# Kernel optimization log

Hardware: AMD Instinct MI355X
Metric: run time of the kernel (lower is better)

Reference implementation:

```python
import jax, jax.numpy as jnp
import numpy as np

HEADS = 8

def setup_inputs() -> dict:
    key = jax.random.key(0)
    k1, k2, k3 = jax.random.split(key, 3)
    B, C, L = 8, 512, 4096
    dim_head = 64
    hidden = HEADS * dim_head  # 512
    x = jax.random.normal(k1, (B, C, L), dtype=jnp.float32)
    # Conv1d(dim, hidden*3, 1, bias=False) -> weight [hidden*3, dim]
    w_qkv = jax.random.normal(k2, (hidden * 3, C), dtype=jnp.float32) * 0.02
    # Conv1d(hidden, dim, 1) -> weight [dim, hidden], bias [dim]
    w_out = jax.random.normal(k3, (C, hidden), dtype=jnp.float32) * 0.02
    b_out = jnp.zeros((C,), dtype=jnp.float32)
    return {"x": x, "w_qkv": w_qkv, "w_out": w_out, "b_out": b_out}

def reference(x, w_qkv, w_out, b_out):
    B, C, L = x.shape
    # 1x1 Conv1d == channel matmul
    qkv = jnp.einsum('oc,bcl->bol', w_qkv, x)            # [B, 3*H*dh, L]
    qkv = qkv.reshape(B, 3, HEADS, -1, L)                # qkv outermost, then heads, then c
    q, k, v = qkv[:, 0], qkv[:, 1], qkv[:, 2]            # each [B, H, dh, L]
    k = jax.nn.softmax(k, axis=-1)                       # softmax over sequence
    context = jnp.einsum('bhdn,bhen->bhde', k, v)        # [B, H, dh, dh]
    out = jnp.einsum('bhde,bhdn->bhen', context, q)      # [B, H, dh, L]
    out = out.reshape(B, -1, L)                          # [B, H*dh, L]
    return jnp.einsum('oc,bcl->bol', w_out, out) + b_out[None, :, None]
```

## Files before the change

kernel.cpp:

```cpp
#include <hip/hip_runtime.h>
#include <hip/hip_bf16.h>


typedef __bf16 bf16x8 __attribute__((ext_vector_type(8)));
typedef __bf16 bf16x4 __attribute__((ext_vector_type(4)));
typedef float  f32x4  __attribute__((ext_vector_type(4)));

#define B_  8
#define L_  4096
#define C_  512

#define GLD_LDS16(g, l)                                             \
    __builtin_amdgcn_global_load_lds(                               \
        (const __attribute__((address_space(1))) void*)(g),         \
        (__attribute__((address_space(3))) void*)(l), 16, 0, 0)

__global__ __launch_bounds__(256) void prep_all(const float* __restrict__ x,
                                                __hip_bfloat16* __restrict__ xt,
                                                const float* __restrict__ wqkv_f,
                                                __hip_bfloat16* __restrict__ wkv_b,
                                                __hip_bfloat16* __restrict__ wqT,
                                                float* __restrict__ ctx) {
    __shared__ float tile[64 * 132];
    int blk = blockIdx.x;
    int t = threadIdx.x;
    if (blk < 2048) {
        int b = blk >> 8, rem = blk & 255;
        int l0 = (rem & 31) * 128, c0 = (rem >> 5) * 64;
        const float* xp = x + ((size_t)b * C_ + c0) * L_ + l0;
#pragma unroll
        for (int p = 0; p < 8; p++) {
            int i = p * 8 + (t >> 5);
            int j = (t & 31) * 4;
            float4 vv = *(const float4*)(xp + (size_t)i * L_ + j);
            *(float4*)&tile[i * 132 + j] = vv;
        }
        __syncthreads();
        unsigned short* xo = (unsigned short*)xt + ((size_t)b * L_ + l0) * C_ + c0;
#pragma unroll
        for (int qq = 0; qq < 8; qq++) {
            int l = qq * 16 + (t >> 4);
            int cg = (t & 15) * 4;
            bf16x4 ov;
#pragma unroll
            for (int k = 0; k < 4; k++) ov[k] = (__bf16)tile[(cg + k) * 132 + l];
            *(bf16x4*)(xo + (size_t)l * C_ + cg) = ov;
        }
    } else if (blk < 4096) {
        int i = (blk - 2048) * 256 + t;
        wkv_b[i] = __float2bfloat16(wqkv_f[512 * 512 + i]);
    } else if (blk < 4352) {
        int tb = blk - 4096;
        int r0 = (tb >> 4) * 32, c0 = (tb & 15) * 32;
        int tx = t & 31, ty = t >> 5;
        for (int r = 0; r < 32; r += 8)
            tile[(ty + r) * 33 + tx] = wqkv_f[(size_t)(r0 + ty + r) * 512 + c0 + tx];
        __syncthreads();
        for (int r = 0; r < 32; r += 8)
            wqT[(size_t)(c0 + ty + r) * 512 + r0 + tx] = __float2bfloat16(tile[tx * 33 + ty + r]);
    } else {
        int i = (blk - 4352) * 256 + t;
        ctx[i] = 0.f;
    }
}

template <int MODE>
__global__ __launch_bounds__(256) void gemm_bt(
    const __hip_bfloat16* __restrict__ A, const __hip_bfloat16* __restrict__ Bt,
    size_t strideA, size_t strideB, int M, int N, int K,
    __hip_bfloat16* __restrict__ kb, __hip_bfloat16* __restrict__ vb,
    __hip_bfloat16* __restrict__ obf,
    float* __restrict__ outb, const float* __restrict__ bias) {
    __shared__ alignas(16) unsigned short As[128 * 64];
    __shared__ alignas(16) unsigned short Bs[128 * 64];

    int b = blockIdx.z;
    int m0 = blockIdx.y * 128, n0 = blockIdx.x * 128;
    const __hip_bfloat16* Ab = A + strideA * (size_t)b;
    const __hip_bfloat16* Bb = Bt + strideB * (size_t)b;

    int t = threadIdx.x;
    int lane = t & 63, wv = t >> 6;
    int l16 = lane & 15, q4 = lane >> 4;
    int wr = (wv >> 1) * 64, wc = (wv & 1) * 64;

    int srow = lane >> 3;
    int swz  = ((lane & 7) ^ srow) * 8;

    const __hip_bfloat16* gA[4];
    const __hip_bfloat16* gB[4];
    unsigned short* lA[4];
    unsigned short* lB[4];
#pragma unroll
    for (int c = 0; c < 4; c++) {
        int r = wv * 32 + c * 8;
        gA[c] = Ab + (size_t)(m0 + r + srow) * K + swz;
        gB[c] = Bb + (size_t)(n0 + r + srow) * K + swz;
        lA[c] = &As[r * 64];
        lB[c] = &Bs[r * 64];
    }

    int gsel0 = ((q4) ^ (l16 & 7)) * 8;
    int gsel1 = ((4 + q4) ^ (l16 & 7)) * 8;
    int rA = (wr + l16) * 64;
    int rB = (wc + l16) * 64;

    f32x4 acc[4][4] = {};

    for (int k0 = 0; k0 < K; k0 += 64) {
        __syncthreads();
#pragma unroll
        for (int c = 0; c < 4; c++) {
            GLD_LDS16(gA[c] + k0, lA[c]);
            GLD_LDS16(gB[c] + k0, lB[c]);
        }
        __syncthreads();

        bf16x8 af[4], bfr[4];
#pragma unroll
        for (int i = 0; i < 4; i++) {
            af[i]  = *(const bf16x8*)&As[rA + i * 1024 + gsel0];
            bfr[i] = *(const bf16x8*)&Bs[rB + i * 1024 + gsel0];
        }
#pragma unroll
        for (int i = 0; i < 4; i++)
#pragma unroll
            for (int j = 0; j < 4; j++)
                acc[i][j] = __builtin_amdgcn_mfma_f32_16x16x32_bf16(af[i], bfr[j], acc[i][j], 0, 0, 0);
#pragma unroll
        for (int i = 0; i < 4; i++) {
            af[i]  = *(const bf16x8*)&As[rA + i * 1024 + gsel1];
            bfr[i] = *(const bf16x8*)&Bs[rB + i * 1024 + gsel1];
        }
#pragma unroll
        for (int i = 0; i < 4; i++)
#pragma unroll
            for (int j = 0; j < 4; j++)
                acc[i][j] = __builtin_amdgcn_mfma_f32_16x16x32_bf16(af[i], bfr[j], acc[i][j], 0, 0, 0);
    }

#pragma unroll
    for (int i = 0; i < 4; i++)
#pragma unroll
        for (int j = 0; j < 4; j++)
#pragma unroll
            for (int r = 0; r < 4; r++) {
                int row = m0 + wr + i * 16 + q4 * 4 + r;
                int col = n0 + wc + j * 16 + l16;
                float val = acc[i][j][r];
                if (MODE == 1) {
                    int part = row >> 9, od = row & 511;
                    size_t idx = ((size_t)b * 512 + od) * (size_t)N + col;
                    __hip_bfloat16 cv = __float2bfloat16(val);
                    if (part == 0) kb[idx] = cv;
                    else           vb[idx] = cv;
                } else if (MODE == 3) {
                    obf[((size_t)b * 512 + row) * (size_t)N + col] = __float2bfloat16(val);
                } else {
                    outb[((size_t)b * 512 + row) * (size_t)N + col] = val + bias[row];
                }
            }
}

__global__ __launch_bounds__(256) void rowstat(const __hip_bfloat16* __restrict__ kin,
                                               float* __restrict__ mrow,
                                               float* __restrict__ isrow) {
    int row = blockIdx.x;
    const unsigned short* kp = (const unsigned short*)kin + (size_t)row * L_;
    __shared__ float buf[L_];
    __shared__ float red[8];
    int t = threadIdx.x, lane = t & 63, wv = t >> 6;
    float m = -1e30f;
    for (int i0 = t * 8; i0 < L_; i0 += 256 * 8) {
        bf16x8 kv = *(const bf16x8*)(kp + i0);
#pragma unroll
        for (int j = 0; j < 8; j++) {
            float xx = (float)kv[j];
            buf[i0 + j] = xx;
            m = fmaxf(m, xx);
        }
    }
    for (int o = 32; o; o >>= 1) m = fmaxf(m, __shfl_xor(m, o, 64));
    if (lane == 0) red[wv] = m;
    __syncthreads();
    m = fmaxf(fmaxf(red[0], red[1]), fmaxf(red[2], red[3]));
    float s = 0.f;
    for (int i = t; i < L_; i += 256) s += __expf(buf[i] - m);
    for (int o = 32; o; o >>= 1) s += __shfl_xor(s, o, 64);
    if (lane == 0) red[4 + wv] = s;
    __syncthreads();
    if (t == 0) {
        s = red[4] + red[5] + red[6] + red[7];
        mrow[row] = m;
        isrow[row] = 1.0f / s;
    }
}

__global__ __launch_bounds__(256) void ctx_kernel(const __hip_bfloat16* __restrict__ kraw,
                                                  const float* __restrict__ mrow,
                                                  const float* __restrict__ isrow,
                                                  const __hip_bfloat16* __restrict__ v,
                                                  float* __restrict__ ctx) {
    int kc = blockIdx.x, h = blockIdx.y, b = blockIdx.z;
    int t = threadIdx.x, lane = t & 63, wv = t >> 6;
    int l16 = lane & 15, q4 = lane >> 4;
    const __hip_bfloat16* ka = kraw + ((size_t)b * 512 + h * 64) * L_;
    const __hip_bfloat16* va = v + ((size_t)b * 512 + h * 64) * L_;
    int rbase = b * 512 + h * 64;
    float mr[4], ir[4];
#pragma unroll
    for (int i = 0; i < 4; i++) {
        mr[i] = mrow[rbase + i * 16 + l16];
        ir[i] = isrow[rbase + i * 16 + l16];
    }
    f32x4 acc[4][4] = {};
    int nbase = kc * 512 + wv * 128;
#pragma unroll
    for (int s = 0; s < 4; s++) {
        int n = nbase + s * 32 + q4 * 8;
        bf16x8 af[4], bfr[4];
#pragma unroll
        for (int i = 0; i < 4; i++) {
            bf16x8 kv = *(const bf16x8*)(ka + (size_t)(i * 16 + l16) * L_ + n);
#pragma unroll
            for (int e = 0; e < 8; e++)
                af[i][e] = (__bf16)(__expf((float)kv[e] - mr[i]) * ir[i]);
            bfr[i] = *(const bf16x8*)(va + (size_t)(i * 16 + l16) * L_ + n);
        }
#pragma unroll
        for (int i = 0; i < 4; i++)
#pragma unroll
            for (int j = 0; j < 4; j++)
                acc[i][j] = __builtin_amdgcn_mfma_f32_16x16x32_bf16(af[i], bfr[j], acc[i][j], 0, 0, 0);
    }
    __shared__ float cbuf[4096];
    for (int w = 0; w < 4; w++) {
        if (wv == w) {
#pragma unroll
            for (int i = 0; i < 4; i++)
#pragma unroll
                for (int j = 0; j < 4; j++)
#pragma unroll
                    for (int r = 0; r < 4; r++) {
                        int mm = i * 16 + q4 * 4 + r, nn = j * 16 + l16;
                        float pv = acc[i][j][r];
                        if (w == 0) cbuf[mm * 64 + nn] = pv;
                        else        cbuf[mm * 64 + nn] += pv;
                    }
        }
        __syncthreads();
    }
    float* cg = ctx + ((size_t)b * 8 + h) * 4096;
    for (int i = t; i < 4096; i += 256) atomicAdd(&cg[i], cbuf[i]);
}

__global__ __launch_bounds__(256) void w2_kernel(const float* __restrict__ wout,
                                                 const float* __restrict__ ctx,
                                                 __hip_bfloat16* __restrict__ w2) {
    int ob = blockIdx.x, h = blockIdx.y, b = blockIdx.z;
    __shared__ float cT[64 * 65];
    __shared__ float wT[64 * 65];
    int t = threadIdx.x;
    const float* cg = ctx + ((size_t)b * 8 + h) * 4096;
    for (int i = t; i < 4096; i += 256) {
        int d = i >> 6, e = i & 63;
        cT[e * 65 + d] = cg[i];
        wT[e * 65 + d] = wout[(size_t)(ob * 64 + d) * 512 + h * 64 + e];
    }
    __syncthreads();
    int ol = t >> 2;
    int db = (t & 3) * 16;
    for (int dd = 0; dd < 16; dd++) {
        int d = db + dd;
        float s = 0.f;
#pragma unroll
        for (int e = 0; e < 64; e++) s += wT[e * 65 + ol] * cT[e * 65 + d];
        w2[((size_t)b * 512 + ob * 64 + ol) * 512 + h * 64 + d] = __float2bfloat16(s);
    }
}

extern "C" void kernel_launch(void* const* d_in, const int* in_sizes, int n_in,
                              void* d_out, int out_size, void* d_ws, size_t ws_size,
                              hipStream_t stream) {
    const float* x     = (const float*)d_in[0];
    const float* w_qkv = (const float*)d_in[1];
    const float* w_out = (const float*)d_in[2];
    const float* b_out = (const float*)d_in[3];
    float* out = (float*)d_out;
    char* ws = (char*)d_ws;

    const size_t QKV = (size_t)B_ * 512 * L_;
    size_t off_xt  = 0;
    size_t off_wkv = off_xt + (size_t)B_ * L_ * C_ * 2;
    size_t off_wqT = off_wkv + (size_t)1024 * 512 * 2;
    size_t off_k   = off_wqT + (size_t)512 * 512 * 2;
    size_t off_v   = off_k + QKV * 2;
    size_t off_ms  = off_v + QKV * 2;
    size_t off_is  = off_ms + 4096 * 4;
    size_t off_ctx = off_is + 4096 * 4;
    size_t off_w2  = off_ctx + (size_t)B_ * 8 * 64 * 64 * 4;
    size_t off_w3  = off_w2 + (size_t)B_ * 512 * 512 * 2;

    __hip_bfloat16* xt   = (__hip_bfloat16*)(ws + off_xt);
    __hip_bfloat16* wkvb = (__hip_bfloat16*)(ws + off_wkv);
    __hip_bfloat16* wqT  = (__hip_bfloat16*)(ws + off_wqT);
    __hip_bfloat16* kb   = (__hip_bfloat16*)(ws + off_k);
    __hip_bfloat16* vb   = (__hip_bfloat16*)(ws + off_v);
    float*          ms   = (float*)(ws + off_ms);
    float*          isv  = (float*)(ws + off_is);
    float*          ctx  = (float*)(ws + off_ctx);
    __hip_bfloat16* w2   = (__hip_bfloat16*)(ws + off_w2);
    __hip_bfloat16* W3   = (__hip_bfloat16*)(ws + off_w3);

    prep_all<<<5376, 256, 0, stream>>>(x, xt, w_qkv, wkvb, wqT, ctx);

    gemm_bt<1><<<dim3(L_ / 128, 1024 / 128, B_), 256, 0, stream>>>(
        wkvb, xt, 0, (size_t)L_ * C_, 1024, L_, 512, kb, vb, nullptr, nullptr, nullptr);

    rowstat<<<B_ * 512, 256, 0, stream>>>(kb, ms, isv);
    ctx_kernel<<<dim3(8, 8, B_), 256, 0, stream>>>(kb, ms, isv, vb, ctx);
    w2_kernel<<<dim3(8, 8, B_), 256, 0, stream>>>(w_out, ctx, w2);

    gemm_bt<3><<<dim3(512 / 128, 512 / 128, B_), 256, 0, stream>>>(
        w2, wqT, (size_t)512 * 512, 0, 512, 512, 512, nullptr, nullptr, W3, nullptr, nullptr);

    gemm_bt<2><<<dim3(L_ / 128, 512 / 128, B_), 256, 0, stream>>>(
        W3, xt, (size_t)512 * 512, (size_t)L_ * C_, 512, L_, 512, nullptr, nullptr, nullptr, out, b_out);
}
```

Measured before the change: 263.2 us.

## Use 256x256-tile double-buffered 8-wave GEMM for QKV and output projections

```diff
diff --git a/kernel.cpp b/kernel.cpp
--- a/kernel.cpp
+++ b/kernel.cpp
@@ -14,6 +14,11 @@
     __builtin_amdgcn_global_load_lds(                               \
         (const __attribute__((address_space(1))) void*)(g),         \
         (__attribute__((address_space(3))) void*)(l), 16, 0, 0)
+
+#define FENCE asm volatile("" ::: "memory")
+#define BAR   do { FENCE; __builtin_amdgcn_s_barrier(); FENCE; } while (0)
+#define DRAIN_LGKM asm volatile("s_waitcnt lgkmcnt(0)" ::: "memory")
+#define WAIT_VM(N) asm volatile("s_waitcnt vmcnt(" #N ")" ::: "memory")
 
 __global__ __launch_bounds__(256) void prep_all(const float* __restrict__ x,
                                                 __hip_bfloat16* __restrict__ xt,
@@ -68,9 +73,7 @@
 __global__ __launch_bounds__(256) void gemm_bt(
     const __hip_bfloat16* __restrict__ A, const __hip_bfloat16* __restrict__ Bt,
     size_t strideA, size_t strideB, int M, int N, int K,
-    __hip_bfloat16* __restrict__ kb, __hip_bfloat16* __restrict__ vb,
-    __hip_bfloat16* __restrict__ obf,
-    float* __restrict__ outb, const float* __restrict__ bias) {
+    __hip_bfloat16* __restrict__ obf) {
     __shared__ alignas(16) unsigned short As[128 * 64];
     __shared__ alignas(16) unsigned short Bs[128 * 64];
 
@@ -147,19 +150,190 @@
             for (int r = 0; r < 4; r++) {
                 int row = m0 + wr + i * 16 + q4 * 4 + r;
                 int col = n0 + wc + j * 16 + l16;
-                float val = acc[i][j][r];
-                if (MODE == 1) {
-                    int part = row >> 9, od = row & 511;
-                    size_t idx = ((size_t)b * 512 + od) * (size_t)N + col;
-                    __hip_bfloat16 cv = __float2bfloat16(val);
-                    if (part == 0) kb[idx] = cv;
-                    else           vb[idx] = cv;
-                } else if (MODE == 3) {
-                    obf[((size_t)b * 512 + row) * (size_t)N + col] = __float2bfloat16(val);
-                } else {
-                    outb[((size_t)b * 512 + row) * (size_t)N + col] = val + bias[row];
+                obf[((size_t)b * 512 + row) * (size_t)N + col] = __float2bfloat16(acc[i][j][r]);
+            }
+}
+
+template <int MODE>
+__global__ __launch_bounds__(512, 2) void gemm256(
+    const __hip_bfloat16* __restrict__ A, const __hip_bfloat16* __restrict__ Bt,
+    size_t strideA, size_t strideB, int M, int N, int K,
+    __hip_bfloat16* __restrict__ kb, __hip_bfloat16* __restrict__ vb,
+    float* __restrict__ outb, const float* __restrict__ bias) {
+    __shared__ alignas(16) unsigned short sA[2][256 * 64];
+    __shared__ alignas(16) unsigned short sB[2][256 * 64];
+
+    int b = blockIdx.z;
+    int m0 = blockIdx.y * 256, n0 = blockIdx.x * 256;
+    const __hip_bfloat16* Ab = A + strideA * (size_t)b;
+    const __hip_bfloat16* Bb = Bt + strideB * (size_t)b;
+
+    int t = threadIdx.x;
+    int lane = t & 63, wv = t >> 6;
+    int l16 = lane & 15, q4 = lane >> 4;
+    int wm = wv >> 2, wn = wv & 3;
+
+    int srow = lane >> 3;
+    int swz  = ((lane & 7) ^ srow) * 8;
+
+    const __hip_bfloat16* gA[4];
+    const __hip_bfloat16* gB[4];
+    unsigned ldoff[4];
+#pragma unroll
+    for (int c = 0; c < 4; c++) {
+        gA[c] = Ab + (size_t)(m0 + c * 64 + wv * 8 + srow) * K + swz;
+        gB[c] = Bb + (size_t)(n0 + c * 64 + wv * 8 + srow) * K + swz;
+        ldoff[c] = (unsigned)(c * 64 + wv * 8) * 64;
+    }
+
+    int gsel0 = (q4 ^ (l16 & 7)) * 8;
+    int gsel1 = gsel0 ^ 32;
+    unsigned offA = (unsigned)(wm * 128 + l16) * 64;
+    unsigned offB = (unsigned)(wn * 64 + l16) * 64;
+    int NKT = K >> 6;
+
+    f32x4 acc[8][4] = {};
+    bf16x8 aF[4][2], bF[4][2];
+
+#pragma unroll
+    for (int c = 0; c < 4; c++) GLD_LDS16(gA[c], &sA[0][ldoff[c]]);
+#pragma unroll
+    for (int c = 0; c < 4; c++) GLD_LDS16(gB[c], &sB[0][ldoff[c]]);
+    if (NKT > 1) {
+        GLD_LDS16(gA[0] + 64, &sA[1][ldoff[0]]);
+        GLD_LDS16(gA[1] + 64, &sA[1][ldoff[1]]);
+        WAIT_VM(2);
+    } else {
+        WAIT_VM(0);
+    }
+    BAR;
+
+#pragma unroll 1
+    for (int kt = 0; kt < NKT; ++kt) {
+        const unsigned short* As_b = sA[kt & 1];
+        const unsigned short* Bs_b = sB[kt & 1];
+        int nbuf = (kt + 1) & 1;
+        int koff1 = (kt + 1) << 6;
+        bool st1 = (kt + 1) < NKT;
+        bool st2 = (kt + 2) < NKT;
+
+#pragma unroll
+        for (int i = 0; i < 4; i++) {
+            aF[i][0] = *(const bf16x8*)&As_b[offA + i * 1024 + gsel0];
+            aF[i][1] = *(const bf16x8*)&As_b[offA + i * 1024 + gsel1];
+        }
+#pragma unroll
+        for (int j = 0; j < 2; j++) {
+            bF[j][0] = *(const bf16x8*)&Bs_b[offB + j * 1024 + gsel0];
+            bF[j][1] = *(const bf16x8*)&Bs_b[offB + j * 1024 + gsel1];
+        }
+        if (st1) {
+            GLD_LDS16(gA[2] + koff1, &sA[nbuf][ldoff[2]]);
+            GLD_LDS16(gA[3] + koff1, &sA[nbuf][ldoff[3]]);
+        }
+        BAR;
+        __builtin_amdgcn_s_setprio(1);
+#pragma unroll
+        for (int ks = 0; ks < 2; ks++)
+#pragma unroll
+            for (int i = 0; i < 4; i++)
+#pragma unroll
+                for (int j = 0; j < 2; j++)
+                    acc[i][j] = __builtin_amdgcn_mfma_f32_16x16x32_bf16(aF[i][ks], bF[j][ks], acc[i][j], 0, 0, 0);
+        __builtin_amdgcn_s_setprio(0);
+        DRAIN_LGKM;
+        BAR;
+
+#pragma unroll
+        for (int j = 2; j < 4; j++) {
+            bF[j][0] = *(const bf16x8*)&Bs_b[offB + j * 1024 + gsel0];
+            bF[j][1] = *(const bf16x8*)&Bs_b[offB + j * 1024 + gsel1];
+        }
+        if (st1) {
+            GLD_LDS16(gB[0] + koff1, &sB[nbuf][ldoff[0]]);
+            GLD_LDS16(gB[1] + koff1, &sB[nbuf][ldoff[1]]);
+        }
+        BAR;
+        __builtin_amdgcn_s_setprio(1);
+#pragma unroll
+        for (int ks = 0; ks < 2; ks++)
+#pragma unroll
+            for (int i = 0; i < 4; i++)
+#pragma unroll
+                for (int j = 0; j < 2; j++)
+                    acc[i][2 + j] = __builtin_amdgcn_mfma_f32_16x16x32_bf16(aF[i][ks], bF[2 + j][ks], acc[i][2 + j], 0, 0, 0);
+        __builtin_amdgcn_s_setprio(0);
+        DRAIN_LGKM;
+        BAR;
+
+#pragma unroll
+        for (int i = 0; i < 4; i++) {
+            aF[i][0] = *(const bf16x8*)&As_b[offA + 4096 + i * 1024 + gsel0];
+            aF[i][1] = *(const bf16x8*)&As_b[offA + 4096 + i * 1024 + gsel1];
+        }
+        if (st1) {
+            GLD_LDS16(gB[2] + koff1, &sB[nbuf][ldoff[2]]);
+            GLD_LDS16(gB[3] + koff1, &sB[nbuf][ldoff[3]]);
+        }
+        BAR;
+        __builtin_amdgcn_s_setprio(1);
+#pragma unroll
+        for (int ks = 0; ks < 2; ks++)
+#pragma unroll
+            for (int i = 0; i < 4; i++)
+#pragma unroll
+                for (int j = 0; j < 2; j++)
+                    acc[4 + i][j] = __builtin_amdgcn_mfma_f32_16x16x32_bf16(aF[i][ks], bF[j][ks], acc[4 + i][j], 0, 0, 0);
+        __builtin_amdgcn_s_setprio(0);
+        DRAIN_LGKM;
+        BAR;
+
+        if (st2) {
+            int koff2 = (kt + 2) << 6;
+            GLD_LDS16(gA[0] + koff2, &sA[kt & 1][ldoff[0]]);
+            GLD_LDS16(gA[1] + koff2, &sA[kt & 1][ldoff[1]]);
+        }
+        BAR;
+        __builtin_amdgcn_s_setprio(1);
+#pragma unroll
+        for (int ks = 0; ks < 2; ks++)
+#pragma unroll
+            for (int i = 0; i < 4; i++)
+#pragma unroll
+                for (int j = 0; j < 2; j++)
+                    acc[4 + i][2 + j] = __builtin_amdgcn_mfma_f32_16x16x32_bf16(aF[i][ks], bF[2 + j][ks], acc[4 + i][2 + j], 0, 0, 0);
+        __builtin_amdgcn_s_setprio(0);
+        DRAIN_LGKM;
+        if (st2) { WAIT_VM(2); } else { WAIT_VM(0); }
+        BAR;
+    }
+
+    int row0 = m0 + wm * 128, col0 = n0 + wn * 64;
+    if (MODE == 1) {
+        __hip_bfloat16* dst = (row0 < 512) ? kb : vb;
+        int ob = row0 & 511;
+#pragma unroll
+        for (int i = 0; i < 8; i++)
+#pragma unroll
+            for (int j = 0; j < 4; j++)
+#pragma unroll
+                for (int r = 0; r < 4; r++) {
+                    int od  = ob + i * 16 + q4 * 4 + r;
+                    int col = col0 + j * 16 + l16;
+                    dst[((size_t)b * 512 + od) * (size_t)N + col] = __float2bfloat16(acc[i][j][r]);
                 }
-            }
+    } else {
+#pragma unroll
+        for (int i = 0; i < 8; i++)
+#pragma unroll
+            for (int j = 0; j < 4; j++)
+#pragma unroll
+                for (int r = 0; r < 4; r++) {
+                    int row = row0 + i * 16 + q4 * 4 + r;
+                    int col = col0 + j * 16 + l16;
+                    outb[((size_t)b * M + row) * (size_t)N + col] = acc[i][j][r] + bias[row];
+                }
+    }
 }
 
 __global__ __launch_bounds__(256) void rowstat(const __hip_bfloat16* __restrict__ kin,
@@ -314,16 +488,16 @@
 
     prep_all<<<5376, 256, 0, stream>>>(x, xt, w_qkv, wkvb, wqT, ctx);
 
-    gemm_bt<1><<<dim3(L_ / 128, 1024 / 128, B_), 256, 0, stream>>>(
-        wkvb, xt, 0, (size_t)L_ * C_, 1024, L_, 512, kb, vb, nullptr, nullptr, nullptr);
+    gemm256<1><<<dim3(L_ / 256, 1024 / 256, B_), 512, 0, stream>>>(
+        wkvb, xt, 0, (size_t)L_ * C_, 1024, L_, 512, kb, vb, nullptr, nullptr);
 
     rowstat<<<B_ * 512, 256, 0, stream>>>(kb, ms, isv);
     ctx_kernel<<<dim3(8, 8, B_), 256, 0, stream>>>(kb, ms, isv, vb, ctx);
     w2_kernel<<<dim3(8, 8, B_), 256, 0, stream>>>(w_out, ctx, w2);
 
     gemm_bt<3><<<dim3(512 / 128, 512 / 128, B_), 256, 0, stream>>>(
-        w2, wqT, (size_t)512 * 512, 0, 512, 512, 512, nullptr, nullptr, W3, nullptr, nullptr);
-
-    gemm_bt<2><<<dim3(L_ / 128, 512 / 128, B_), 256, 0, stream>>>(
-        W3, xt, (size_t)512 * 512, (size_t)L_ * C_, 512, L_, 512, nullptr, nullptr, nullptr, out, b_out);
-}
+        w2, wqT, (size_t)512 * 512, 0, 512, 512, 512, W3);
+
+    gemm256<2><<<dim3(L_ / 256, 512 / 256, B_), 512, 0, stream>>>(
+        W3, xt, (size_t)512 * 512, (size_t)L_ * C_, 512, L_, 512, nullptr, nullptr, out, b_out);
+}
```

Measured after the change: 258.0 us. -2.0%, faster.
